# Kernel tuning notes

Hardware: AMD Instinct MI355X
Metric: run time of the kernel (lower is better)

## Reference

```python
import jax, jax.numpy as jnp
import numpy as np

HS = 2048   # hidden_size
NH = 16     # num_attention_heads
HD = HS // NH  # head_dim = 128
FD = 256    # feature_dim
EPS = 1e-5  # layer_norm_epsilon


def setup_inputs() -> dict:
    key = jax.random.key(0)
    ks = jax.random.split(key, 12)
    s = 0.02
    return {
        "hidden_states": jax.random.normal(ks[0], (2, 4096, HS), jnp.float32),
        "attention_mask": jnp.zeros((2, 4096), jnp.float32),
        "Wq": jax.random.normal(ks[1], (HS, HS), jnp.float32) * s,
        "bq": jnp.zeros((HS,), jnp.float32),
        "Wk": jax.random.normal(ks[2], (HS, HS), jnp.float32) * s,
        "bk": jnp.zeros((HS,), jnp.float32),
        "Wv": jax.random.normal(ks[3], (HS, HS), jnp.float32) * s,
        "bv": jnp.zeros((HS,), jnp.float32),
        "Wo": jax.random.normal(ks[4], (HS, HS), jnp.float32) * s,
        "bo": jnp.zeros((HS,), jnp.float32),
        "Wf1": jax.random.normal(ks[5], (HD, FD), jnp.float32) * s,
        "bf1": jnp.zeros((FD,), jnp.float32),
        "Wf2": jax.random.normal(ks[6], (FD, FD), jnp.float32) * s,
        "bf2": jnp.zeros((FD,), jnp.float32),
        "ln_g": jnp.ones((FD,), jnp.float32),
        "ln_b": jnp.zeros((FD,), jnp.float32),
    }


def reference(hidden_states, attention_mask, Wq, bq, Wk, bk, Wv, bv, Wo, bo,
              Wf1, bf1, Wf2, bf2, ln_g, ln_b):
    B, L, H = hidden_states.shape

    # QKV projections -> [B, NH, L, HD]
    q = (hidden_states @ Wq + bq).reshape(B, L, NH, HD).transpose(0, 2, 1, 3)
    k = (hidden_states @ Wk + bk).reshape(B, L, NH, HD).transpose(0, 2, 1, 3)
    v = (hidden_states @ Wv + bv).reshape(B, L, NH, HD).transpose(0, 2, 1, 3)

    # seq_len (4096) > linear_threshold (1024) -> linear attention branch
    def feature_map(x):  # Linear -> ReLU -> Linear -> LayerNorm
        h = jax.nn.relu(x @ Wf1 + bf1)
        h = h @ Wf2 + bf2
        mu = jnp.mean(h, axis=-1, keepdims=True)
        var = jnp.var(h, axis=-1, keepdims=True)  # biased, like torch LayerNorm
        return (h - mu) * jax.lax.rsqrt(var + EPS) * ln_g + ln_b

    q_feat = feature_map(q)  # [B, NH, L, FD]
    k_feat = feature_map(k)
    # attention_mask [B, L] -> k_feat * (1 + mask)
    k_feat = k_feat * (1.0 + attention_mask[:, None, :, None])

    kv = jnp.einsum('bhlf,bhld->bhfd', k_feat, v)          # [B, NH, FD, HD]
    attn = jnp.einsum('bhlf,bhfd->bhld', q_feat, kv)       # [B, NH, L, HD]
    k_sum = jnp.sum(k_feat, axis=2)                         # [B, NH, FD]
    denom = jnp.einsum('bhlf,bhf->bhl', q_feat, k_sum)[..., None]
    attn = attn / (denom + 1e-8)

    attn = attn.transpose(0, 2, 1, 3).reshape(B, L, H)
    return attn @ Wo + bo
```

## Files before the change

kernel.cpp:

```cpp
#include <hip/hip_runtime.h>

typedef unsigned short u16;
typedef unsigned int u32;
typedef __attribute__((ext_vector_type(8))) short bf16x8;
typedef __attribute__((ext_vector_type(4))) float f32x4;

#define B_ 2
#define L_ 4096
#define HS_ 2048
#define NH_ 16
#define HD_ 128
#define FD_ 256

__device__ __forceinline__ float bf2f(u16 u) { return __uint_as_float(((u32)u) << 16); }
__device__ __forceinline__ u16 f2bf(float f) {
    u32 x = __float_as_uint(f);
    return (u16)((x + 0x7fffu + ((x >> 16) & 1u)) >> 16);
}

__device__ __forceinline__ void llds16(const u16* g, u16* l) {
    __builtin_amdgcn_global_load_lds((const __attribute__((address_space(1))) void*)g,
                                     (__attribute__((address_space(3))) void*)l, 16, 0, 0);
}

__device__ __forceinline__ void gemm_mainloop(const u16* __restrict__ Ab, int lda,
                                              const u16* __restrict__ Bb, int ldb,
                                              int K, u16* As, u16* Bs, f32x4 (&acc)[4][4]) {
    const int tid  = threadIdx.x;
    const int lane = tid & 63;
    const int wave = tid >> 6;
    const int wm = wave >> 1, wn = wave & 1;

    f32x4 zero = {0.f, 0.f, 0.f, 0.f};
#pragma unroll
    for (int i = 0; i < 4; i++)
#pragma unroll
        for (int j = 0; j < 4; j++) acc[i][j] = zero;

    const int srow = lane >> 2;
    const int scol = (lane & 3) * 8;
    const u16* pa = Ab + (size_t)(wave * 32 + srow) * lda + scol;
    const u16* pb = Bb + (size_t)(wave * 32 + srow) * ldb + scol;
    u16* la = As + wave * 1024;
    u16* lb = Bs + wave * 1024;

    const int arow = (wm * 64 + (lane & 15)) * 32 + (lane >> 4) * 8;
    const int brow = (wn * 64 + (lane & 15)) * 32 + (lane >> 4) * 8;

    for (int k0 = 0; k0 < K; k0 += 32) {
        llds16(pa, la);
        llds16(pa + 16 * lda, la + 512);
        llds16(pb, lb);
        llds16(pb + 16 * ldb, lb + 512);
        pa += 32; pb += 32;
        __syncthreads();
        bf16x8 af[4], bg[4];
#pragma unroll
        for (int mt = 0; mt < 4; mt++) af[mt] = *(const bf16x8*)(As + arow + mt * 512);
#pragma unroll
        for (int nt = 0; nt < 4; nt++) bg[nt] = *(const bf16x8*)(Bs + brow + nt * 512);
#pragma unroll
        for (int mt = 0; mt < 4; mt++)
#pragma unroll
            for (int nt = 0; nt < 4; nt++)
                acc[mt][nt] = __builtin_amdgcn_mfma_f32_16x16x32_bf16(af[mt], bg[nt], acc[mt][nt], 0, 0, 0);
        __syncthreads();
    }
}

__global__ __launch_bounds__(256) void k_cvt(const float* __restrict__ src, u16* __restrict__ dst) {
    size_t i = ((size_t)blockIdx.x * 256 + threadIdx.x) * 8;
    float4 a = *(const float4*)(src + i);
    float4 b = *(const float4*)(src + i + 4);
    union { u16 h[8]; uint4 v; } o;
    o.h[0] = f2bf(a.x); o.h[1] = f2bf(a.y); o.h[2] = f2bf(a.z); o.h[3] = f2bf(a.w);
    o.h[4] = f2bf(b.x); o.h[5] = f2bf(b.y); o.h[6] = f2bf(b.z); o.h[7] = f2bf(b.w);
    *(uint4*)(dst + i) = o.v;
}

__global__ __launch_bounds__(256) void k_transpose(const float* Wq, const float* Wk, const float* Wv,
                                                   const float* Wo, const float* Wf1, const float* Wf2,
                                                   u16* Wqkv_t, u16* Wo_t, u16* Wf1_t, u16* Wf2_t) {
    const float* src; u16* dst; int R, C;
    switch (blockIdx.z) {
        case 0: src = Wq;  dst = Wqkv_t;                R = 2048; C = 2048; break;
        case 1: src = Wk;  dst = Wqkv_t + 2048 * 2048;  R = 2048; C = 2048; break;
        case 2: src = Wv;  dst = Wqkv_t + 2 * 2048 * 2048; R = 2048; C = 2048; break;
        case 3: src = Wo;  dst = Wo_t;                  R = 2048; C = 2048; break;
        case 4: src = Wf1; dst = Wf1_t;                 R = 128;  C = 256;  break;
        default: src = Wf2; dst = Wf2_t;                R = 256;  C = 256;  break;
    }
    int c0 = blockIdx.x * 32, r0 = blockIdx.y * 32;
    if (c0 >= C || r0 >= R) return;
    __shared__ u16 tile[32][33];
    int tx = threadIdx.x, ty = threadIdx.y;
    for (int i = ty; i < 32; i += 8) tile[i][tx] = f2bf(src[(size_t)(r0 + i) * C + c0 + tx]);
    __syncthreads();
    for (int i = ty; i < 32; i += 8) dst[(size_t)(c0 + i) * R + r0 + tx] = tile[tx][i];
}

#define QKV_BAR() { __builtin_amdgcn_sched_barrier(0); __builtin_amdgcn_s_barrier(); \
                    __builtin_amdgcn_sched_barrier(0); }
#define QKV_LGKM0() { asm volatile("s_waitcnt lgkmcnt(0)" ::: "memory"); \
                      __builtin_amdgcn_sched_barrier(0); }

__device__ __forceinline__ void mainloop256(const u16* __restrict__ Abase,
                                            const u16* __restrict__ Bbase,
                                            u16* LDS, f32x4 (&acc)[8][4]) {
    const int tid = threadIdx.x, lane = tid & 63, wave = tid >> 6;
    const int wm = wave >> 2, wn = wave & 3;

    int r0g, c0g, r1g, c1g;
    { int p = tid * 16; int s = p >> 10, q = p & 1023; q ^= ((q >> 9) & 1) << 5;
      r0g = (s >> 1) * 16 + (q >> 6); c0g = (s & 1) * 32 + ((q & 63) >> 1); }
    { int p = 8192 + tid * 16; int s = p >> 10, q = p & 1023; q ^= ((q >> 9) & 1) << 5;
      r1g = (s >> 1) * 16 + (q >> 6); c1g = (s & 1) * 32 + ((q & 63) >> 1); }
    const int voff0 = r0g * HS_ + c0g;
    const int voff1 = r1g * HS_ + c1g;

    int qby = (lane & 15) * 64 + (lane >> 4) * 16;
    qby ^= ((qby >> 9) & 1) << 5;
    const int qh = qby >> 1;

#define STG(G, soff, dstu) { \
    llds16((G) + (soff) + voff0, LDS + (dstu) + wave * 512); \
    llds16((G) + (soff) + voff1, LDS + (dstu) + 4096 + wave * 512); }

    const size_t a0 = 0, a1 = (size_t)128 * HS_;
    const size_t b0 = 0, b1 = (size_t)128 * HS_;

    STG(Bbase, b0, 32768); STG(Bbase, b1, 40960);
    STG(Abase, a0, 0);     STG(Abase, a1, 8192);
    STG(Bbase, b0 + 64, 49152); STG(Bbase, b1 + 64, 57344);
    STG(Abase, a0 + 64, 16384);
    asm volatile("s_waitcnt vmcnt(6)" ::: "memory");
    QKV_BAR();

    f32x4 zero = {0.f, 0.f, 0.f, 0.f};
#pragma unroll
    for (int i = 0; i < 8; i++)
#pragma unroll
        for (int j = 0; j < 4; j++) acc[i][j] = zero;

    const int NT = HS_ / 64;
    bf16x8 afr[4][2], bfr[4][2];
    for (int t = 0; t < NT; t++) {
        const int bsel = t & 1;
        const u16* Ah = LDS + bsel * 16384 + wm * 8192;
        const u16* Bh = LDS + 32768 + bsel * 16384 + (wn >> 1) * 8192;
        const int bg0 = (wn & 1) * 4;
        const size_t kc1 = (size_t)(t + 1) * 64, kc2 = (size_t)(t + 2) * 64;

#pragma unroll
        for (int mf = 0; mf < 4; mf++)
#pragma unroll
            for (int ks = 0; ks < 2; ks++)
                afr[mf][ks] = *(const bf16x8*)(Ah + (mf * 2 + ks) * 512 + qh);
#pragma unroll
        for (int nf = 0; nf < 4; nf++)
#pragma unroll
            for (int ks = 0; ks < 2; ks++)
                bfr[nf][ks] = *(const bf16x8*)(Bh + ((bg0 + nf) * 2 + ks) * 512 + qh);
        if (t + 1 < NT) STG(Abase, a1 + kc1, (bsel ^ 1) * 16384 + 8192);
        QKV_BAR();
        QKV_LGKM0();
        __builtin_amdgcn_s_setprio(1);
#pragma unroll
        for (int mf = 0; mf < 4; mf++)
#pragma unroll
            for (int nf = 0; nf < 2; nf++)
#pragma unroll
                for (int ks = 0; ks < 2; ks++)
                    acc[mf][nf] = __builtin_amdgcn_mfma_f32_16x16x32_bf16(afr[mf][ks], bfr[nf][ks], acc[mf][nf], 0, 0, 0);
        __builtin_amdgcn_s_setprio(0);
        QKV_BAR();
        if (t + 2 < NT) STG(Bbase, b0 + kc2, 32768 + bsel * 16384);
        QKV_BAR();
        __builtin_amdgcn_s_setprio(1);
#pragma unroll
        for (int mf = 0; mf < 4; mf++)
#pragma unroll
            for (int nf = 2; nf < 4; nf++)
#pragma unroll
                for (int ks = 0; ks < 2; ks++)
                    acc[mf][nf] = __builtin_amdgcn_mfma_f32_16x16x32_bf16(afr[mf][ks], bfr[nf][ks], acc[mf][nf], 0, 0, 0);
        __builtin_amdgcn_s_setprio(0);
        QKV_BAR();
#pragma unroll
        for (int mf = 0; mf < 4; mf++)
#pragma unroll
            for (int ks = 0; ks < 2; ks++)
                afr[mf][ks] = *(const bf16x8*)(Ah + ((mf + 4) * 2 + ks) * 512 + qh);
        if (t + 2 < NT) STG(Bbase, b1 + kc2, 32768 + bsel * 16384 + 8192);
        QKV_BAR();
        QKV_LGKM0();
        __builtin_amdgcn_s_setprio(1);
#pragma unroll
        for (int mf = 0; mf < 4; mf++)
#pragma unroll
            for (int nf = 0; nf < 2; nf++)
#pragma unroll
                for (int ks = 0; ks < 2; ks++)
                    acc[mf + 4][nf] = __builtin_amdgcn_mfma_f32_16x16x32_bf16(afr[mf][ks], bfr[nf][ks], acc[mf + 4][nf], 0, 0, 0);
        __builtin_amdgcn_s_setprio(0);
        QKV_BAR();
        if (t + 2 < NT) STG(Abase, a0 + kc2, bsel * 16384);
        QKV_BAR();
        __builtin_amdgcn_s_setprio(1);
#pragma unroll
        for (int mf = 0; mf < 4; mf++)
#pragma unroll
            for (int nf = 2; nf < 4; nf++)
#pragma unroll
                for (int ks = 0; ks < 2; ks++)
                    acc[mf + 4][nf] = __builtin_amdgcn_mfma_f32_16x16x32_bf16(afr[mf][ks], bfr[nf][ks], acc[mf + 4][nf], 0, 0, 0);
        __builtin_amdgcn_s_setprio(0);
        if (t + 2 < NT) { asm volatile("s_waitcnt vmcnt(6)" ::: "memory"); }
        else if (t + 1 < NT) { asm volatile("s_waitcnt vmcnt(0)" ::: "memory"); }
        QKV_BAR();
    }
#undef STG
}

__global__ __launch_bounds__(512, 2) void k_gemm_qkv(
        const u16* __restrict__ X, const u16* __restrict__ Wt,
        const float* __restrict__ bq, const float* __restrict__ bk, const float* __restrict__ bv,
        u16* __restrict__ qout, u16* __restrict__ kout, u16* __restrict__ vT) {
    __shared__ u16 LDS[65536];
    const int tid = threadIdx.x, lane = tid & 63, wave = tid >> 6;
    const int wm = wave >> 2, wn = wave & 3;

    const int xcd = blockIdx.x & 7, idx = blockIdx.x >> 3;
    const int nblk = idx >> 2;
    const int mblk = xcd * 4 + (idx & 3);
    const int mb = mblk * 256, nb = nblk * 256;

    f32x4 acc[8][4];
    mainloop256(X + (size_t)mb * HS_, Wt + (size_t)nb * HS_, LDS, acc);

    const int which = nblk >> 3;
    const int colbase = (nblk & 7) * 256;
    const int bi = mb >> 12, lb = mb & 4095;
    const float* bias = (which == 0) ? bq : (which == 1 ? bk : bv);
    const int rb = (lane >> 4) << 2, cl = lane & 15;

    if (which < 2) {
        u16* dst = (which == 0) ? qout : kout;
        const int bh0 = bi * NH_ + (colbase >> 7);
        for (int half = 0; half < 2; half++) {
            if (wm == half) {
#pragma unroll
                for (int nf = 0; nf < 4; nf++) {
                    float bvv = bias[colbase + wn * 64 + nf * 16 + cl];
#pragma unroll
                    for (int mf = 0; mf < 8; mf++)
#pragma unroll
                        for (int r = 0; r < 4; r++)
                            LDS[(mf * 16 + rb + r) * 264 + wn * 64 + nf * 16 + cl] =
                                f2bf(acc[mf][nf][r] + bvv);
                }
            }
            __syncthreads();
#pragma unroll
            for (int it = 0; it < 8; it++) {
                int row = (tid >> 5) + it * 16;
                int c8 = (tid & 31) * 8;
                uint2 lo = *(const uint2*)(LDS + row * 264 + c8);
                uint2 hi = *(const uint2*)(LDS + row * 264 + c8 + 4);
                uint4 val = make_uint4(lo.x, lo.y, hi.x, hi.y);
                u16* pp = dst + ((size_t)(bh0 + (c8 >> 7)) * L_ + lb + half * 128 + row) * HD_ + (c8 & 127);
                *(uint4*)pp = val;
            }
            __syncthreads();
        }
    } else {
        for (int half = 0; half < 2; half++) {
            if (wm == half) {
#pragma unroll
                for (int nf = 0; nf < 4; nf++) {
                    float bvv = bias[colbase + wn * 64 + nf * 16 + cl];
#pragma unroll
                    for (int mf = 0; mf < 8; mf++)
#pragma unroll
                        for (int r = 0; r < 4; r++)
                            LDS[(wn * 64 + nf * 16 + cl) * 136 + mf * 16 + rb + r] =
                                f2bf(acc[mf][nf][r] + bvv);
                }
            }
            __syncthreads();
#pragma unroll
            for (int it = 0; it < 8; it++) {
                int n = (tid >> 4) + it * 32;
                int c8 = (tid & 15) * 8;
                uint2 lo = *(const uint2*)(LDS + n * 136 + c8);
                uint2 hi = *(const uint2*)(LDS + n * 136 + c8 + 4);
                uint4 val = make_uint4(lo.x, lo.y, hi.x, hi.y);
                int cg = colbase + n;
                u16* pp = vT + ((size_t)(bi * NH_ + (cg >> 7)) * HD_ + (cg & 127)) * L_ + lb + half * 128 + c8;
                *(uint4*)pp = val;
            }
            __syncthreads();
        }
    }
}

__global__ __launch_bounds__(512, 2) void k_gemm_out(const u16* __restrict__ A, const u16* __restrict__ Wt,
                                                     const float* __restrict__ bo, float* __restrict__ out) {
    __shared__ u16 LDS[65536];
    const int lane = threadIdx.x & 63, wave = threadIdx.x >> 6;
    const int wm = wave >> 2, wn = wave & 3;

    const int xcd = blockIdx.x & 7, idx = blockIdx.x >> 3;
    const int nblk = idx >> 2;
    const int mblk = xcd * 4 + (idx & 3);
    const int mb = mblk * 256, nb = nblk * 256;

    f32x4 acc[8][4];
    mainloop256(A + (size_t)mb * HS_, Wt + (size_t)nb * HS_, LDS, acc);

    const int rb = (lane >> 4) << 2, cl = lane & 15;
#pragma unroll
    for (int nf = 0; nf < 4; nf++) {
        int n = nb + wn * 64 + nf * 16 + cl;
        float bvv = bo[n];
#pragma unroll
        for (int mf = 0; mf < 8; mf++) {
            int m = mb + wm * 128 + mf * 16 + rb;
#pragma unroll
            for (int r = 0; r < 4; r++)
                out[(size_t)(m + r) * HS_ + n] = acc[mf][nf][r] + bvv;
        }
    }
}

template <int MASKED, int TRANS>
__global__ __launch_bounds__(256) void k_feat(const u16* __restrict__ X,
                                              const u16* __restrict__ W1t, const float* __restrict__ b1,
                                              const u16* __restrict__ W2t, const float* __restrict__ b2,
                                              const float* __restrict__ g, const float* __restrict__ be,
                                              const float* __restrict__ mask, const float* __restrict__ ksum,
                                              const u16* __restrict__ kvT,
                                              u16* __restrict__ feat, float* __restrict__ ksp,
                                              u16* __restrict__ attnOut) {
    __shared__ u16 As[64 * 32];
    __shared__ u16 Bs[256 * 32];
    __shared__ u16 H[64 * 264];
    __shared__ float MU[64], RS[64], FAC[64], RD[64];
    const int tid = threadIdx.x, lane = tid & 63, wave = tid >> 6;
    const int mb = blockIdx.x * 64;

    const int srow = lane >> 2, scol = (lane & 3) * 8;
    const int arow_rd = (lane & 15);
    const int kgrp = (lane >> 4) * 8;

    f32x4 acc[4][4];
    f32x4 zero = {0.f, 0.f, 0.f, 0.f};
#pragma unroll
    for (int i = 0; i < 4; i++)
#pragma unroll
        for (int j = 0; j < 4; j++) acc[i][j] = zero;

    for (int k0 = 0; k0 < 128; k0 += 32) {
        llds16(X + (size_t)(mb + wave * 16 + srow) * 128 + k0 + scol, As + wave * 512);
#pragma unroll
        for (int i = 0; i < 4; i++)
            llds16(W1t + (size_t)((wave * 4 + i) * 16 + srow) * 128 + k0 + scol,
                   Bs + (wave * 4 + i) * 512);
        __syncthreads();
        bf16x8 af[4], bg[4];
#pragma unroll
        for (int mt = 0; mt < 4; mt++) af[mt] = *(const bf16x8*)(As + (mt * 16 + arow_rd) * 32 + kgrp);
#pragma unroll
        for (int nt = 0; nt < 4; nt++) bg[nt] = *(const bf16x8*)(Bs + (wave * 64 + nt * 16 + arow_rd) * 32 + kgrp);
#pragma unroll
        for (int mt = 0; mt < 4; mt++)
#pragma unroll
            for (int nt = 0; nt < 4; nt++)
                acc[mt][nt] = __builtin_amdgcn_mfma_f32_16x16x32_bf16(af[mt], bg[nt], acc[mt][nt], 0, 0, 0);
        __syncthreads();
    }
    {
        const int rbase = (lane >> 4) << 2;
#pragma unroll
        for (int nt = 0; nt < 4; nt++) {
            int n = wave * 64 + nt * 16 + (lane & 15);
            float bvv = b1[n];
#pragma unroll
            for (int mt = 0; mt < 4; mt++)
#pragma unroll
                for (int r = 0; r < 4; r++) {
                    float v = fmaxf(acc[mt][nt][r] + bvv, 0.f);
                    H[(mt * 16 + rbase + r) * 264 + n] = f2bf(v);
                }
            acc[0][nt] = zero; acc[1][nt] = zero; acc[2][nt] = zero; acc[3][nt] = zero;
        }
    }
    __syncthreads();

    for (int k0 = 0; k0 < 256; k0 += 32) {
#pragma unroll
        for (int i = 0; i < 4; i++)
            llds16(W2t + (size_t)((wave * 4 + i) * 16 + srow) * 256 + k0 + scol,
                   Bs + (wave * 4 + i) * 512);
        __syncthreads();
        bf16x8 af[4], bg[4];
#pragma unroll
        for (int mt = 0; mt < 4; mt++) af[mt] = *(const bf16x8*)(H + (mt * 16 + arow_rd) * 264 + k0 + kgrp);
#pragma unroll
        for (int nt = 0; nt < 4; nt++) bg[nt] = *(const bf16x8*)(Bs + (wave * 64 + nt * 16 + arow_rd) * 32 + kgrp);
#pragma unroll
        for (int mt = 0; mt < 4; mt++)
#pragma unroll
            for (int nt = 0; nt < 4; nt++)
                acc[mt][nt] = __builtin_amdgcn_mfma_f32_16x16x32_bf16(af[mt], bg[nt], acc[mt][nt], 0, 0, 0);
        __syncthreads();
    }
    {
        const int rbase = (lane >> 4) << 2;
#pragma unroll
        for (int nt = 0; nt < 4; nt++) {
            int n = wave * 64 + nt * 16 + (lane & 15);
            float bvv = b2[n];
#pragma unroll
            for (int mt = 0; mt < 4; mt++)
#pragma unroll
                for (int r = 0; r < 4; r++)
                    H[(mt * 16 + rbase + r) * 264 + n] = f2bf(acc[mt][nt][r] + bvv);
        }
    }
    __syncthreads();

    {
        for (int r = 0; r < 16; r++) {
            int row = wave * 16 + r;
            int j = lane * 4;
            uint2 u = *(const uint2*)(H + row * 264 + j);
            float x0 = bf2f((u16)(u.x & 0xffff)), x1 = bf2f((u16)(u.x >> 16));
            float x2 = bf2f((u16)(u.y & 0xffff)), x3 = bf2f((u16)(u.y >> 16));
            float s = x0 + x1 + x2 + x3;
            float ss = x0 * x0 + x1 * x1 + x2 * x2 + x3 * x3;
#pragma unroll
            for (int o = 32; o >= 1; o >>= 1) { s += __shfl_xor(s, o); ss += __shfl_xor(ss, o); }
            if (lane == 0) {
                float mu = s * (1.f / FD_);
                float var = ss * (1.f / FD_) - mu * mu;
                MU[row] = mu;
                RS[row] = rsqrtf(var + 1e-5f);
                float fac = 1.f;
                if (MASKED) {
                    int grow = mb + row;
                    int b = grow >> 16;
                    int l = grow & 4095;
                    fac = 1.f + mask[b * L_ + l];
                }
                FAC[row] = fac;
            }
        }
    }
    __syncthreads();

    if (!TRANS) {
        const int bh = mb >> 12;
        {
            int j = lane * 4;
            float4 gg = *(const float4*)(g + j);
            float4 bb = *(const float4*)(be + j);
            float4 kk = *(const float4*)(ksum + (size_t)bh * FD_ + j);
            for (int r = 0; r < 16; r++) {
                int row = wave * 16 + r;
                float mu = MU[row], rstd = RS[row], fac = FAC[row];
                uint2 u = *(const uint2*)(H + row * 264 + j);
                float x0 = bf2f((u16)(u.x & 0xffff)), x1 = bf2f((u16)(u.x >> 16));
                float x2 = bf2f((u16)(u.y & 0xffff)), x3 = bf2f((u16)(u.y >> 16));
                u16 h0 = f2bf(((x0 - mu) * rstd * gg.x + bb.x) * fac);
                u16 h1 = f2bf(((x1 - mu) * rstd * gg.y + bb.y) * fac);
                u16 h2 = f2bf(((x2 - mu) * rstd * gg.z + bb.z) * fac);
                u16 h3 = f2bf(((x3 - mu) * rstd * gg.w + bb.w) * fac);
                uint2 o2;
                o2.x = (u32)h0 | ((u32)h1 << 16);
                o2.y = (u32)h2 | ((u32)h3 << 16);
                *(uint2*)(H + row * 264 + j) = o2;
                float dp = bf2f(h0) * kk.x + bf2f(h1) * kk.y + bf2f(h2) * kk.z + bf2f(h3) * kk.w;
#pragma unroll
                for (int o = 32; o >= 1; o >>= 1) dp += __shfl_xor(dp, o);
                if (lane == 0) RD[row] = 1.f / (dp + 1e-8f);
            }
        }
        const u16* kvTb = kvT + (size_t)bh * HD_ * FD_;
        f32x4 pacc[8];
#pragma unroll
        for (int i = 0; i < 8; i++) pacc[i] = zero;
        for (int k0 = 0; k0 < 256; k0 += 32) {
            llds16(kvTb + (size_t)(wave * 32 + srow) * FD_ + k0 + scol, Bs + (wave * 32) * 32);
            llds16(kvTb + (size_t)(wave * 32 + 16 + srow) * FD_ + k0 + scol, Bs + (wave * 32 + 16) * 32);
            __syncthreads();
            bf16x8 af = *(const bf16x8*)(H + (wave * 16 + arow_rd) * 264 + k0 + kgrp);
#pragma unroll
            for (int nt = 0; nt < 8; nt++) {
                bf16x8 bg = *(const bf16x8*)(Bs + (nt * 16 + arow_rd) * 32 + kgrp);
                pacc[nt] = __builtin_amdgcn_mfma_f32_16x16x32_bf16(af, bg, pacc[nt], 0, 0, 0);
            }
            __syncthreads();
        }
        const int rbase = (lane >> 4) << 2, cl = lane & 15;
#pragma unroll
        for (int nt = 0; nt < 8; nt++)
#pragma unroll
            for (int r = 0; r < 4; r++) {
                int row = wave * 16 + rbase + r;
                H[row * 264 + nt * 16 + cl] = f2bf(pacc[nt][r] * RD[row]);
            }
        __syncthreads();
        const int b = bh >> 4, h = bh & 15, lb = mb & 4095;
        const int c8 = (tid & 15) * 8;
#pragma unroll
        for (int it = 0; it < 4; it++) {
            int row = (tid >> 4) + it * 16;
            uint2 lo = *(const uint2*)(H + row * 264 + c8);
            uint2 hi = *(const uint2*)(H + row * 264 + c8 + 4);
            *(uint4*)(attnOut + ((size_t)(b * L_ + lb + row)) * HS_ + h * HD_ + c8) =
                make_uint4(lo.x, lo.y, hi.x, hi.y);
        }
    } else {
        int f = tid;
        int bh = mb >> 12, lb = mb & 4095;
        float gf = g[f], bf = be[f];
        u16* orow = feat + ((size_t)bh * FD_ + f) * L_ + lb;
        float fsum = 0.f;
        for (int lg = 0; lg < 64; lg += 8) {
            union { u16 h8[8]; uint4 v4; } pk;
#pragma unroll
            for (int j = 0; j < 8; j++) {
                int row = lg + j;
                float x = bf2f(H[row * 264 + f]);
                float y = ((x - MU[row]) * RS[row] * gf + bf) * FAC[row];
                fsum += y;
                pk.h8[j] = f2bf(y);
            }
            *(uint4*)(orow + lg) = pk.v4;
        }
        ksp[((size_t)bh * 64 + (lb >> 6)) * FD_ + f] = fsum;
    }
}

__global__ __launch_bounds__(256) void k_ksum2(const float* __restrict__ ksp, float* __restrict__ ksum) {
    const int bh = blockIdx.x, f = threadIdx.x;
    float s = 0.f;
    for (int i = 0; i < 64; i++) s += ksp[((size_t)bh * 64 + i) * FD_ + f];
    ksum[(size_t)bh * FD_ + f] = s;
}

__global__ __launch_bounds__(256) void k_gemm_kv(const u16* __restrict__ kfT, const u16* __restrict__ vT,
                                                 float* __restrict__ kvp) {
    __shared__ u16 As[4096], Bs[4096];
    f32x4 acc[4][4];
    const int mb = blockIdx.x * 128;
    const int ks = blockIdx.y;
    const int bh = blockIdx.z;
    gemm_mainloop(kfT + ((size_t)bh * FD_ + mb) * L_ + ks * 1024, L_,
                  vT + (size_t)bh * HD_ * L_ + ks * 1024, L_, 1024, As, Bs, acc);
    const int lane = threadIdx.x & 63, wave = threadIdx.x >> 6;
    const int wm = wave >> 1, wn = wave & 1;
    const int n0 = wn * 64 + (lane & 15);
    const int m0 = mb + wm * 64 + ((lane >> 4) << 2);
    float* o = kvp + (size_t)(ks * 32 + bh) * (FD_ * HD_);
#pragma unroll
    for (int nt = 0; nt < 4; nt++)
#pragma unroll
        for (int mt = 0; mt < 4; mt++)
#pragma unroll
            for (int r = 0; r < 4; r++)
                o[(size_t)(m0 + mt * 16 + r) * HD_ + n0 + nt * 16] = acc[mt][nt][r];
}

__global__ __launch_bounds__(256) void k_kvred(const float* __restrict__ kvp, u16* __restrict__ kvT) {
    const int p = blockIdx.x, bh = blockIdx.y, t = threadIdx.x;
    const int e0 = p * 4096 + t * 16;
    float s[16];
#pragma unroll
    for (int i = 0; i < 16; i++) s[i] = 0.f;
    for (int c = 0; c < 4; c++) {
        const float* src = kvp + ((size_t)(c * 32 + bh)) * 32768 + e0;
#pragma unroll
        for (int i = 0; i < 16; i += 4) {
            float4 vv = *(const float4*)(src + i);
            s[i] += vv.x; s[i + 1] += vv.y; s[i + 2] += vv.z; s[i + 3] += vv.w;
        }
    }
#pragma unroll
    for (int i = 0; i < 16; i++) {
        int e = e0 + i, fq = e >> 7, d = e & 127;
        kvT[((size_t)bh * HD_ + d) * FD_ + fq] = f2bf(s[i]);
    }
}

extern "C" void kernel_launch(void* const* d_in, const int* in_sizes, int n_in,
                              void* d_out, int out_size, void* d_ws, size_t ws_size,
                              hipStream_t stream) {
    const float* hs  = (const float*)d_in[0];
    const float* msk = (const float*)d_in[1];
    const float* Wq  = (const float*)d_in[2];  const float* bq  = (const float*)d_in[3];
    const float* Wk  = (const float*)d_in[4];  const float* bk  = (const float*)d_in[5];
    const float* Wv  = (const float*)d_in[6];  const float* bv  = (const float*)d_in[7];
    const float* Wo  = (const float*)d_in[8];  const float* bo  = (const float*)d_in[9];
    const float* Wf1 = (const float*)d_in[10]; const float* bf1 = (const float*)d_in[11];
    const float* Wf2 = (const float*)d_in[12]; const float* bf2 = (const float*)d_in[13];
    const float* lng = (const float*)d_in[14]; const float* lnb = (const float*)d_in[15];
    float* out = (float*)d_out;
    char* w = (char*)d_ws;

    u16* Wqkv_t = (u16*)(w + 0);
    u16* Xbf    = (u16*)(w + 25165824u);
    u16* kfT    = (u16*)(w + 67108864u);
    u16* qbuf   = (u16*)(w + 134217728u);
    u16* kbuf   = (u16*)(w + 167772160u);
    float* kvp  = (float*)(w + 167772160u);
    u16* attn   = (u16*)(w + 167772160u);
    u16* vT     = (u16*)(w + 201326592u);
    u16* Wo_t   = (u16*)(w + 234881024u);
    u16* Wf1_t  = (u16*)(w + 243269632u);
    u16* Wf2_t  = (u16*)(w + 243335168u);
    float* ksp  = (float*)(w + 243466240u);
    u16* kvT    = (u16*)(w + 245563392u);
    float* ksum = (float*)(w + 247660544u);

    k_cvt<<<dim3(8192), 256, 0, stream>>>(hs, Xbf);
    k_transpose<<<dim3(64, 64, 6), dim3(32, 8), 0, stream>>>(Wq, Wk, Wv, Wo, Wf1, Wf2,
                                                             Wqkv_t, Wo_t, Wf1_t, Wf2_t);
    k_gemm_qkv<<<dim3(768), 512, 0, stream>>>(Xbf, Wqkv_t, bq, bk, bv, qbuf, kbuf, vT);
    k_feat<1, 1><<<dim3(2048), 256, 0, stream>>>(kbuf, Wf1_t, bf1, Wf2_t, bf2, lng, lnb, msk,
                                                 nullptr, nullptr, kfT, ksp, nullptr);
    k_ksum2<<<dim3(32), 256, 0, stream>>>(ksp, ksum);
    k_gemm_kv<<<dim3(2, 4, 32), 256, 0, stream>>>(kfT, vT, kvp);
    k_kvred<<<dim3(8, 32), 256, 0, stream>>>(kvp, kvT);
    k_feat<0, 0><<<dim3(2048), 256, 0, stream>>>(qbuf, Wf1_t, bf1, Wf2_t, bf2, lng, lnb, msk,
                                                 ksum, kvT, nullptr, nullptr, attn);
    k_gemm_out<<<dim3(256), 512, 0, stream>>>(attn, Wo_t, bo, out);
}
```

Baseline: 673.1 us.

## Double-buffer LDS tiles in GEMM mainloop and feature-map kernel

Converts the shared GEMM mainloop and the k_feat kernel's three MFMA loops to double-buffered LDS staging. The next K-tile is prefetched via global_load_lds while the current tile is consumed, and the first tile of the following stage (W2t, kvT) is prefetched during the last iteration of the previous one. This aims to hide global-load latency behind MFMA work and drop one barrier per iteration. In exchange it doubles LDS usage, which can lower occupancy, and it relies on correct barrier placement around the buffer swaps.

```diff
diff --git a/kernel.cpp b/kernel.cpp
--- a/kernel.cpp
+++ b/kernel.cpp
@@ -41,24 +41,35 @@
     const int scol = (lane & 3) * 8;
     const u16* pa = Ab + (size_t)(wave * 32 + srow) * lda + scol;
     const u16* pb = Bb + (size_t)(wave * 32 + srow) * ldb + scol;
-    u16* la = As + wave * 1024;
-    u16* lb = Bs + wave * 1024;
 
     const int arow = (wm * 64 + (lane & 15)) * 32 + (lane >> 4) * 8;
     const int brow = (wn * 64 + (lane & 15)) * 32 + (lane >> 4) * 8;
 
+    llds16(pa, As + wave * 1024);
+    llds16(pa + 16 * lda, As + wave * 1024 + 512);
+    llds16(pb, Bs + wave * 1024);
+    llds16(pb + 16 * ldb, Bs + wave * 1024 + 512);
+    pa += 32; pb += 32;
+    __syncthreads();
+
     for (int k0 = 0; k0 < K; k0 += 32) {
-        llds16(pa, la);
-        llds16(pa + 16 * lda, la + 512);
-        llds16(pb, lb);
-        llds16(pb + 16 * ldb, lb + 512);
-        pa += 32; pb += 32;
-        __syncthreads();
+        const int cur = (k0 >> 5) & 1;
+        u16* Ac = As + cur * 4096;
+        u16* Bc = Bs + cur * 4096;
+        if (k0 + 32 < K) {
+            u16* An = As + (cur ^ 1) * 4096;
+            u16* Bn = Bs + (cur ^ 1) * 4096;
+            llds16(pa, An + wave * 1024);
+            llds16(pa + 16 * lda, An + wave * 1024 + 512);
+            llds16(pb, Bn + wave * 1024);
+            llds16(pb + 16 * ldb, Bn + wave * 1024 + 512);
+            pa += 32; pb += 32;
+        }
         bf16x8 af[4], bg[4];
 #pragma unroll
-        for (int mt = 0; mt < 4; mt++) af[mt] = *(const bf16x8*)(As + arow + mt * 512);
-#pragma unroll
-        for (int nt = 0; nt < 4; nt++) bg[nt] = *(const bf16x8*)(Bs + brow + nt * 512);
+        for (int mt = 0; mt < 4; mt++) af[mt] = *(const bf16x8*)(Ac + arow + mt * 512);
+#pragma unroll
+        for (int nt = 0; nt < 4; nt++) bg[nt] = *(const bf16x8*)(Bc + brow + nt * 512);
 #pragma unroll
         for (int mt = 0; mt < 4; mt++)
 #pragma unroll
@@ -342,8 +353,8 @@
                                               const u16* __restrict__ kvT,
                                               u16* __restrict__ feat, float* __restrict__ ksp,
                                               u16* __restrict__ attnOut) {
-    __shared__ u16 As[64 * 32];
-    __shared__ u16 Bs[256 * 32];
+    __shared__ u16 As[2][2048];
+    __shared__ u16 Bs[2][8192];
     __shared__ u16 H[64 * 264];
     __shared__ float MU[64], RS[64], FAC[64], RD[64];
     const int tid = threadIdx.x, lane = tid & 63, wave = tid >> 6;
@@ -360,18 +371,32 @@
 #pragma unroll
         for (int j = 0; j < 4; j++) acc[i][j] = zero;
 
-    for (int k0 = 0; k0 < 128; k0 += 32) {
-        llds16(X + (size_t)(mb + wave * 16 + srow) * 128 + k0 + scol, As + wave * 512);
-#pragma unroll
-        for (int i = 0; i < 4; i++)
-            llds16(W1t + (size_t)((wave * 4 + i) * 16 + srow) * 128 + k0 + scol,
-                   Bs + (wave * 4 + i) * 512);
-        __syncthreads();
+    llds16(X + (size_t)(mb + wave * 16 + srow) * 128 + scol, As[0] + wave * 512);
+#pragma unroll
+    for (int i = 0; i < 4; i++)
+        llds16(W1t + (size_t)((wave * 4 + i) * 16 + srow) * 128 + scol, Bs[0] + (wave * 4 + i) * 512);
+    __syncthreads();
+#pragma unroll
+    for (int t = 0; t < 4; t++) {
+        const int cur = t & 1;
+        if (t < 3) {
+            const int k1 = (t + 1) * 32;
+            llds16(X + (size_t)(mb + wave * 16 + srow) * 128 + k1 + scol, As[cur ^ 1] + wave * 512);
+#pragma unroll
+            for (int i = 0; i < 4; i++)
+                llds16(W1t + (size_t)((wave * 4 + i) * 16 + srow) * 128 + k1 + scol,
+                       Bs[cur ^ 1] + (wave * 4 + i) * 512);
+        } else {
+#pragma unroll
+            for (int i = 0; i < 4; i++)
+                llds16(W2t + (size_t)((wave * 4 + i) * 16 + srow) * 256 + scol,
+                       Bs[0] + (wave * 4 + i) * 512);
+        }
         bf16x8 af[4], bg[4];
 #pragma unroll
-        for (int mt = 0; mt < 4; mt++) af[mt] = *(const bf16x8*)(As + (mt * 16 + arow_rd) * 32 + kgrp);
-#pragma unroll
-        for (int nt = 0; nt < 4; nt++) bg[nt] = *(const bf16x8*)(Bs + (wave * 64 + nt * 16 + arow_rd) * 32 + kgrp);
+        for (int mt = 0; mt < 4; mt++) af[mt] = *(const bf16x8*)(As[cur] + (mt * 16 + arow_rd) * 32 + kgrp);
+#pragma unroll
+        for (int nt = 0; nt < 4; nt++) bg[nt] = *(const bf16x8*)(Bs[cur] + (wave * 64 + nt * 16 + arow_rd) * 32 + kgrp);
 #pragma unroll
         for (int mt = 0; mt < 4; mt++)
 #pragma unroll
@@ -397,17 +422,26 @@
     }
     __syncthreads();
 
-    for (int k0 = 0; k0 < 256; k0 += 32) {
-#pragma unroll
-        for (int i = 0; i < 4; i++)
-            llds16(W2t + (size_t)((wave * 4 + i) * 16 + srow) * 256 + k0 + scol,
-                   Bs + (wave * 4 + i) * 512);
-        __syncthreads();
+#pragma unroll
+    for (int t = 0; t < 8; t++) {
+        const int cur = t & 1;
+        if (t < 7) {
+            const int k1 = (t + 1) * 32;
+#pragma unroll
+            for (int i = 0; i < 4; i++)
+                llds16(W2t + (size_t)((wave * 4 + i) * 16 + srow) * 256 + k1 + scol,
+                       Bs[cur ^ 1] + (wave * 4 + i) * 512);
+        } else if (!TRANS) {
+            const u16* kvTb = kvT + (size_t)(mb >> 12) * HD_ * FD_;
+            llds16(kvTb + (size_t)(wave * 32 + srow) * FD_ + scol, Bs[0] + wave * 1024);
+            llds16(kvTb + (size_t)(wave * 32 + 16 + srow) * FD_ + scol, Bs[0] + wave * 1024 + 512);
+        }
+        const int k0 = t * 32;
         bf16x8 af[4], bg[4];
 #pragma unroll
         for (int mt = 0; mt < 4; mt++) af[mt] = *(const bf16x8*)(H + (mt * 16 + arow_rd) * 264 + k0 + kgrp);
 #pragma unroll
-        for (int nt = 0; nt < 4; nt++) bg[nt] = *(const bf16x8*)(Bs + (wave * 64 + nt * 16 + arow_rd) * 32 + kgrp);
+        for (int nt = 0; nt < 4; nt++) bg[nt] = *(const bf16x8*)(Bs[cur] + (wave * 64 + nt * 16 + arow_rd) * 32 + kgrp);
 #pragma unroll
         for (int mt = 0; mt < 4; mt++)
 #pragma unroll
@@ -461,6 +495,7 @@
 
     if (!TRANS) {
         const int bh = mb >> 12;
+        const u16* kvTb = kvT + (size_t)bh * HD_ * FD_;
         {
             int j = lane * 4;
             float4 gg = *(const float4*)(g + j);
@@ -486,18 +521,23 @@
                 if (lane == 0) RD[row] = 1.f / (dp + 1e-8f);
             }
         }
-        const u16* kvTb = kvT + (size_t)bh * HD_ * FD_;
+        __syncthreads();
         f32x4 pacc[8];
 #pragma unroll
         for (int i = 0; i < 8; i++) pacc[i] = zero;
-        for (int k0 = 0; k0 < 256; k0 += 32) {
-            llds16(kvTb + (size_t)(wave * 32 + srow) * FD_ + k0 + scol, Bs + (wave * 32) * 32);
-            llds16(kvTb + (size_t)(wave * 32 + 16 + srow) * FD_ + k0 + scol, Bs + (wave * 32 + 16) * 32);
-            __syncthreads();
+#pragma unroll
+        for (int t = 0; t < 8; t++) {
+            const int cur = t & 1;
+            if (t < 7) {
+                const int k1 = (t + 1) * 32;
+                llds16(kvTb + (size_t)(wave * 32 + srow) * FD_ + k1 + scol, Bs[cur ^ 1] + wave * 1024);
+                llds16(kvTb + (size_t)(wave * 32 + 16 + srow) * FD_ + k1 + scol, Bs[cur ^ 1] + wave * 1024 + 512);
+            }
+            const int k0 = t * 32;
             bf16x8 af = *(const bf16x8*)(H + (wave * 16 + arow_rd) * 264 + k0 + kgrp);
 #pragma unroll
             for (int nt = 0; nt < 8; nt++) {
-                bf16x8 bg = *(const bf16x8*)(Bs + (nt * 16 + arow_rd) * 32 + kgrp);
+                bf16x8 bg = *(const bf16x8*)(Bs[cur] + (nt * 16 + arow_rd) * 32 + kgrp);
                 pacc[nt] = __builtin_amdgcn_mfma_f32_16x16x32_bf16(af, bg, pacc[nt], 0, 0, 0);
             }
             __syncthreads();
@@ -552,7 +592,7 @@
 
 __global__ __launch_bounds__(256) void k_gemm_kv(const u16* __restrict__ kfT, const u16* __restrict__ vT,
                                                  float* __restrict__ kvp) {
-    __shared__ u16 As[4096], Bs[4096];
+    __shared__ u16 As[8192], Bs[8192];
     f32x4 acc[4][4];
     const int mb = blockIdx.x * 128;
     const int ks = blockIdx.y;
```

After: 679.5 us. Within noise of the previous version (+1.0%).
